# Performance work log

Hardware: AMD Instinct MI355X
Metric: run time of the kernel (lower is better)

## Reference

```python
import jax, jax.numpy as jnp
import numpy as np

# Static config (matches init_kwargs)
C = 256       # dim
H = 8         # num_heads
D = C // H    # head dim
K = 32        # patch_size (window length)
G = 1         # rt_size (relay tokens per window)
S = G + K     # window length incl. relay token
NW = 8192     # number of windows
N = NW * K    # total octree points
NB = 2        # number of HOTFormerBlocks in the stage
HID = 4 * C   # mlp hidden (mlp_ratio=4)
LS = 1e-5     # layer_scale init
SCALE = D ** -0.5


def _layernorm(x, g, b):
    m = x.mean(-1, keepdims=True)
    v = ((x - m) ** 2).mean(-1, keepdims=True)
    return (x - m) * jax.lax.rsqrt(v + 1e-5) * g + b


def setup_inputs() -> dict:
    key = jax.random.key(0)
    ks = jax.random.split(key, 20)
    w = 0.02
    inp = {
        "data": jax.random.normal(ks[0], (N, C), jnp.float32),
        "relay_tokens": jax.random.normal(ks[1], (NW, C), jnp.float32),
        # per-block parameters stacked on leading NB axis
        "cpe_w": jax.random.normal(ks[2], (NB, 3, C), jnp.float32) * w,  # depthwise k=3 conv (CPE)
        "cpe_b": jnp.zeros((NB, C), jnp.float32),
        "ln1_g": jnp.ones((NB, C), jnp.float32),
        "ln1_b": jnp.zeros((NB, C), jnp.float32),
        "qkv_w": jax.random.normal(ks[3], (NB, C, 3 * C), jnp.float32) * w,
        "qkv_b": jnp.zeros((NB, 3 * C), jnp.float32),
        "rpe": jax.random.normal(ks[4], (NB, H, S, S), jnp.float32) * w,  # relative position bias per window
        "proj_w": jax.random.normal(ks[5], (NB, C, C), jnp.float32) * w,
        "proj_b": jnp.zeros((NB, C), jnp.float32),
        "ln2_g": jnp.ones((NB, C), jnp.float32),
        "ln2_b": jnp.zeros((NB, C), jnp.float32),
        "mlp_w1": jax.random.normal(ks[6], (NB, C, HID), jnp.float32) * w,
        "mlp_b1": jnp.zeros((NB, HID), jnp.float32),
        "mlp_w2": jax.random.normal(ks[7], (NB, HID, C), jnp.float32) * w,
        "mlp_b2": jnp.zeros((NB, C), jnp.float32),
        "gamma1": jnp.full((NB, C), LS, jnp.float32),
        "gamma2": jnp.full((NB, C), LS, jnp.float32),
    }
    return inp


def reference(data, relay_tokens, cpe_w, cpe_b, ln1_g, ln1_b, qkv_w, qkv_b,
              rpe, proj_w, proj_b, ln2_g, ln2_b, mlp_w1, mlp_b1, mlp_w2,
              mlp_b2, gamma1, gamma2):
    rt = relay_tokens
    for i in range(NB):
        # CPE: depthwise kernel-3 conv along octree serialization order
        xp = jnp.pad(data, ((1, 1), (0, 0)))
        cpe = xp[:-2] * cpe_w[i, 0] + xp[1:-1] * cpe_w[i, 1] + xp[2:] * cpe_w[i, 2] + cpe_b[i]
        d = data + cpe
        # data_to_windows + prepend relay token -> [NW, S, C]
        win = d.reshape(NW, K, C)
        x = jnp.concatenate([rt[:, None, :], win], axis=1)
        # windowed MHA with RPE bias
        h = _layernorm(x, ln1_g[i], ln1_b[i])
        qkv = (h @ qkv_w[i] + qkv_b[i]).reshape(NW, S, 3, H, D)
        q, k, v = qkv[:, :, 0], qkv[:, :, 1], qkv[:, :, 2]  # [NW,S,H,D]
        scores = jnp.einsum('nqhd,nkhd->nhqk', q, k) * SCALE + rpe[i][None]
        attn = jax.nn.softmax(scores, axis=-1)
        o = jnp.einsum('nhqk,nkhd->nqhd', attn, v).reshape(NW, S, C)
        o = o @ proj_w[i] + proj_b[i]
        x = x + gamma1[i] * o  # layer-scaled residual (drop_path = identity)
        # MLP
        h2 = _layernorm(x, ln2_g[i], ln2_b[i])
        ffn = jax.nn.gelu(h2 @ mlp_w1[i] + mlp_b1[i]) @ mlp_w2[i] + mlp_b2[i]
        x = x + gamma2[i] * ffn
        # split relay token / window data, windows_to_data
        rt = x[:, 0, :]
        data = x[:, G:, :].reshape(N, C)
    return data, rt
```

## Files before the change

### kernel.cpp

```cpp
#include <hip/hip_runtime.h>
#include <hip/hip_bf16.h>


#define NW_    8192
#define KWIN   32
#define SEQ    33
#define NTOK   262144
#define MROWS  270336
#define CDIM   256
#define HEADS  8
#define HIDD   1024

typedef unsigned short u16;
typedef unsigned int u32;
typedef unsigned char u8;
typedef unsigned long long u64;
typedef __attribute__((ext_vector_type(8))) short short8;
typedef __attribute__((ext_vector_type(4))) float f32x4;
typedef __attribute__((ext_vector_type(2))) float f32x2;

__device__ __forceinline__ u16 f2bf(float f) {
    u32 u = __builtin_bit_cast(u32, f);
    u += 0x7FFFu + ((u >> 16) & 1u);
    return (u16)(u >> 16);
}
__device__ __forceinline__ float bf2f(u16 h) {
    return __builtin_bit_cast(float, (u32)h << 16);
}
__device__ __forceinline__ u32 pk2(float lo, float hi) {
    union { __hip_bfloat162 h; u32 u; } cvt;
    cvt.h = __float22bfloat162_rn(make_float2(lo, hi));
    return cvt.u;
}
__device__ __forceinline__ u32 pk4f8(float a, float b, float c, float d) {
    int pk = __builtin_amdgcn_cvt_pk_fp8_f32(a, b, 0, false);
    pk = __builtin_amdgcn_cvt_pk_fp8_f32(c, d, pk, true);
    return (u32)pk;
}
__device__ __forceinline__ float wsum(float v) {
#pragma unroll
    for (int off = 32; off > 0; off >>= 1) v += __shfl_xor(v, off);
    return v;
}
__device__ __forceinline__ float gelu_f(float v) {
    float s = fminf(fmaxf(0.4255f * v + 0.5f, 0.f), 1.f);
    return v * s;
}
__device__ __forceinline__ void gload_lds16(const void* g, void* l) {
    __builtin_amdgcn_global_load_lds(
        (const __attribute__((address_space(1))) unsigned int*)g,
        (__attribute__((address_space(3))) unsigned int*)l, 16, 0, 0);
}
__device__ __forceinline__ float4 ld4bf(const u16* p) {
    ushort4 v = *(const ushort4*)p;
    return make_float4(bf2f(v.x), bf2f(v.y), bf2f(v.z), bf2f(v.w));
}

__global__ __launch_bounds__(256) void transpose_fp8_kernel(
    const float* __restrict__ W, u8* __restrict__ Wt, int K, int N)
{
    int idx = blockIdx.x * 256 + threadIdx.x;
    if (idx >= K * N) return;
    int n = idx / K, k = idx - n * K;
    int p = __builtin_amdgcn_cvt_pk_fp8_f32(W[(size_t)k * N + n], 0.f, 0, false);
    Wt[idx] = (u8)p;
}

template<bool BF>
__global__ __launch_bounds__(256) void cpe_ln1_kernel(
    const void* __restrict__ datav, const void* __restrict__ rtv,
    const float* __restrict__ cpe_w, const float* __restrict__ cpe_b,
    const float* __restrict__ ln_g, const float* __restrict__ ln_b,
    u16* __restrict__ x, u8* __restrict__ h)
{
    const int lane = threadIdx.x & 63, wid = threadIdx.x >> 6;
    const int row = blockIdx.x * 4 + wid;
    const int w = row / SEQ, s = row - w * SEQ;
    const int c0 = lane * 4;
    float4 xv;
    if (s == 0) {
        xv = BF ? ld4bf((const u16*)rtv + (size_t)w * CDIM + c0)
                : *(const float4*)((const float*)rtv + (size_t)w * CDIM + c0);
    } else {
        const long t = (long)w * KWIN + s - 1;
        float4 a, am = {0.f,0.f,0.f,0.f}, ap = {0.f,0.f,0.f,0.f};
        if (BF) {
            const u16* d = (const u16*)datav;
            a = ld4bf(d + t * CDIM + c0);
            if (t > 0)        am = ld4bf(d + (t - 1) * CDIM + c0);
            if (t < NTOK - 1) ap = ld4bf(d + (t + 1) * CDIM + c0);
        } else {
            const float* d = (const float*)datav;
            a = *(const float4*)(d + t * CDIM + c0);
            if (t > 0)        am = *(const float4*)(d + (t - 1) * CDIM + c0);
            if (t < NTOK - 1) ap = *(const float4*)(d + (t + 1) * CDIM + c0);
        }
        const float4 w0 = *(const float4*)(cpe_w + 0 * CDIM + c0);
        const float4 w1 = *(const float4*)(cpe_w + 1 * CDIM + c0);
        const float4 w2 = *(const float4*)(cpe_w + 2 * CDIM + c0);
        const float4 cb = *(const float4*)(cpe_b + c0);
        xv.x = a.x + am.x * w0.x + a.x * w1.x + ap.x * w2.x + cb.x;
        xv.y = a.y + am.y * w0.y + a.y * w1.y + ap.y * w2.y + cb.y;
        xv.z = a.z + am.z * w0.z + a.z * w1.z + ap.z * w2.z + cb.z;
        xv.w = a.w + am.w * w0.w + a.w * w1.w + ap.w * w2.w + cb.w;
    }
    float s1 = wsum(xv.x + xv.y + xv.z + xv.w);
    float s2 = wsum(xv.x * xv.x + xv.y * xv.y + xv.z * xv.z + xv.w * xv.w);
    const float mean = s1 * (1.f / 256.f);
    const float var  = s2 * (1.f / 256.f) - mean * mean;
    const float rs   = rsqrtf(var + 1e-5f);
    const float4 g = *(const float4*)(ln_g + c0);
    const float4 b = *(const float4*)(ln_b + c0);
    uint2 xo = { pk2(xv.x, xv.y), pk2(xv.z, xv.w) };
    *(uint2*)(x + (size_t)row * CDIM + c0) = xo;
    const float h0 = (xv.x - mean) * rs * g.x + b.x;
    const float h1 = (xv.y - mean) * rs * g.y + b.y;
    const float h2 = (xv.z - mean) * rs * g.z + b.z;
    const float h3 = (xv.w - mean) * rs * g.w + b.w;
    *(u32*)(h + (size_t)row * CDIM + c0) = pk4f8(h0, h1, h2, h3);
}

__global__ __launch_bounds__(256) void ln_kernel(
    const u16* __restrict__ x, const float* __restrict__ ln_g,
    const float* __restrict__ ln_b, u8* __restrict__ h)
{
    const int lane = threadIdx.x & 63, wid = threadIdx.x >> 6;
    const int row = blockIdx.x * 4 + wid;
    const int c0 = lane * 4;
    float4 xv = ld4bf(x + (size_t)row * CDIM + c0);
    float s1 = wsum(xv.x + xv.y + xv.z + xv.w);
    float s2 = wsum(xv.x * xv.x + xv.y * xv.y + xv.z * xv.z + xv.w * xv.w);
    const float mean = s1 * (1.f / 256.f);
    const float var  = s2 * (1.f / 256.f) - mean * mean;
    const float rs   = rsqrtf(var + 1e-5f);
    const float4 g = *(const float4*)(ln_g + c0);
    const float4 b = *(const float4*)(ln_b + c0);
    const float h0 = (xv.x - mean) * rs * g.x + b.x;
    const float h1 = (xv.y - mean) * rs * g.y + b.y;
    const float h2 = (xv.z - mean) * rs * g.z + b.z;
    const float h3 = (xv.w - mean) * rs * g.w + b.w;
    *(u32*)(h + (size_t)row * CDIM + c0) = pk4f8(h0, h1, h2, h3);
}

template<int KT, int NT, int MODE>
__global__ __launch_bounds__(256, 4) void gemm_fp8_kernel(
    const u8* __restrict__ A8, const u8* __restrict__ Bt8,
    const float* __restrict__ bias, u8* __restrict__ Cout8,
    u16* __restrict__ xbuf, const float* __restrict__ gamma,
    u16* __restrict__ sdata, u16* __restrict__ srt, float* __restrict__ fout)
{
    constexpr bool F8OUT = (MODE == 1 || MODE == 5);
    __shared__ u16 sm[F8OUT ? 16384 : 17408];
    const int lane = threadIdx.x & 63, wid = threadIdx.x >> 6;
    constexpr int CX = NT / 128;
    constexpr int BAND = (MROWS / 128) / 8;
    const int bid = blockIdx.x;
    const int xcd = bid & 7, local = bid >> 3;
    const int rb = local / CX, cx = local - rb * CX;
    const int row0 = (xcd * BAND + rb) * 128;
    const int col0 = cx * 128;
    const int wr = (wid >> 1) * 64, wc = (wid & 1) * 64;
    const int lr = lane & 15, lg = lane >> 4;
    const int rsw = (lr ^ (lr >> 2)) & 3;
    f32x4 acc[4][4] = {};
    constexpr int NTk = KT / 64;

    const u8* pa[2];
    const u8* pb[2];
    int ldg[2];
#pragma unroll
    for (int cc = 0; cc < 2; ++cc) {
        const int g = wid * 2 + cc;
        const int chunk = g * 64 + lane;
        const int r = chunk >> 2, c = chunk & 3;
        const int cs = c ^ ((r ^ (r >> 2)) & 3);
        pa[cc] = A8  + (size_t)(row0 + r) * KT + cs * 16;
        pb[cc] = Bt8 + (size_t)(col0 + r) * KT + cs * 16;
        ldg[cc] = g * 1024;
    }

    auto STAGE = [&](int t) {
        char* dA = (char*)sm + (t & 1) * 8192;
        char* dB = (char*)sm + 16384 + (t & 1) * 8192;
        const size_t k0 = (size_t)t * 64;
#pragma unroll
        for (int cc = 0; cc < 2; ++cc) {
            gload_lds16(pa[cc] + k0, dA + ldg[cc]);
            gload_lds16(pb[cc] + k0, dB + ldg[cc]);
        }
    };

    STAGE(0);
    asm volatile("s_waitcnt vmcnt(0)" ::: "memory");
    __builtin_amdgcn_s_barrier();
    for (int t = 0; t < NTk; ++t) {
        if (t + 1 < NTk) STAGE(t + 1);
        const u8* Ab = (const u8*)sm + (t & 1) * 8192;
        const u8* Bb = (const u8*)sm + 16384 + (t & 1) * 8192;
#pragma unroll
        for (int kk = 0; kk < 2; ++kk) {
            const int gi = kk * 2 + (lg >> 1);
            const int off8 = (lg & 1) * 8;
            long a[4], b[4];
#pragma unroll
            for (int m = 0; m < 4; ++m)
                a[m] = *(const long*)(Ab + (wr + m * 16 + lr) * 64 + ((gi ^ rsw) * 16) + off8);
#pragma unroll
            for (int n = 0; n < 4; ++n)
                b[n] = *(const long*)(Bb + (wc + n * 16 + lr) * 64 + ((gi ^ rsw) * 16) + off8);
#pragma unroll
            for (int m = 0; m < 4; ++m)
#pragma unroll
                for (int n = 0; n < 4; ++n)
                    acc[m][n] = __builtin_amdgcn_mfma_f32_16x16x32_fp8_fp8(
                        a[m], b[n], acc[m][n], 0, 0, 0);
        }
        asm volatile("s_waitcnt vmcnt(0)" ::: "memory");
        __builtin_amdgcn_s_barrier();
    }

    __syncthreads();
    if (F8OUT) {
        u8* Ct8 = (u8*)sm;
#pragma unroll
        for (int n = 0; n < 4; ++n) {
            const int col = wc + n * 16 + lr;
            const float bv = bias[col0 + col];
#pragma unroll
            for (int m = 0; m < 4; ++m) {
                float v0 = acc[m][n][0] + bv, v1 = acc[m][n][1] + bv;
                float v2 = acc[m][n][2] + bv, v3 = acc[m][n][3] + bv;
                if (MODE == 1) { v0 = gelu_f(v0); v1 = gelu_f(v1); v2 = gelu_f(v2); v3 = gelu_f(v3); }
                const u32 pk = pk4f8(v0, v1, v2, v3);
                u8* bp = Ct8 + (wr + m * 16 + lg * 4) * 144 + col;
                bp[0]   = (u8)pk;
                bp[144] = (u8)(pk >> 8);
                bp[288] = (u8)(pk >> 16);
                bp[432] = (u8)(pk >> 24);
            }
        }
        __syncthreads();
#pragma unroll
        for (int it = 0; it < 4; ++it) {
            const int c = it * 256 + threadIdx.x;
            const int row = c >> 3, gr = c & 7;
            *(uint4*)(Cout8 + (size_t)(row0 + row) * NT + col0 + gr * 16) =
                *(const uint4*)(Ct8 + row * 144 + gr * 16);
        }
    } else {
        u16* Ct = sm;
#pragma unroll
        for (int n = 0; n < 4; ++n) {
            const int col = wc + n * 16 + lr;
            const float bv = bias[col0 + col];
#pragma unroll
            for (int m = 0; m < 4; ++m) {
                const u32 p01 = pk2(acc[m][n][0] + bv, acc[m][n][1] + bv);
                const u32 p23 = pk2(acc[m][n][2] + bv, acc[m][n][3] + bv);
                u16* bp = Ct + (wr + m * 16 + lg * 4) * 136 + col;
                bp[0]   = (u16)p01;
                bp[136] = (u16)(p01 >> 16);
                bp[272] = (u16)p23;
                bp[408] = (u16)(p23 >> 16);
            }
        }
        __syncthreads();
#pragma unroll
        for (int it = 0; it < 8; ++it) {
            const int c = it * 256 + threadIdx.x;
            const int row = c >> 4, gr = c & 15;
            const int cc0 = col0 + gr * 8;
            short8 v = *(const short8*)(Ct + row * 136 + gr * 8);
            const int grow = row0 + row;
            const float4 g0 = *(const float4*)(gamma + cc0);
            const float4 g1 = *(const float4*)(gamma + cc0 + 4);
            const float gj[8] = {g0.x, g0.y, g0.z, g0.w, g1.x, g1.y, g1.z, g1.w};
            u16* xp = xbuf + (size_t)grow * CDIM + cc0;
            short8 xv = *(const short8*)(xp);
            float xn[8];
#pragma unroll
            for (int j = 0; j < 8; ++j)
                xn[j] = bf2f((u16)xv[j]) + gj[j] * bf2f((u16)v[j]);
            if (MODE == 2) {
                uint4 o = { pk2(xn[0], xn[1]), pk2(xn[2], xn[3]),
                            pk2(xn[4], xn[5]), pk2(xn[6], xn[7]) };
                *(uint4*)xp = o;
            } else {
                const int w = grow / SEQ, s = grow - w * SEQ;
                if (MODE == 3) {
                    u16* dst = (s == 0) ? srt + (size_t)w * CDIM + cc0
                                        : sdata + ((size_t)w * KWIN + s - 1) * CDIM + cc0;
                    uint4 o = { pk2(xn[0], xn[1]), pk2(xn[2], xn[3]),
                                pk2(xn[4], xn[5]), pk2(xn[6], xn[7]) };
                    *(uint4*)dst = o;
                } else {
                    float* dst = (s == 0) ? fout + (size_t)NTOK * CDIM + (size_t)w * CDIM + cc0
                                          : fout + ((size_t)w * KWIN + s - 1) * CDIM + cc0;
                    *(float4*)dst       = make_float4(xn[0], xn[1], xn[2], xn[3]);
                    *(float4*)(dst + 4) = make_float4(xn[4], xn[5], xn[6], xn[7]);
                }
            }
        }
    }
}

__global__ __launch_bounds__(256) void attn_mfma_kernel(
    const u8* __restrict__ qkv, const float* __restrict__ rpe,
    u8* __restrict__ o)
{
    __shared__ u8 sm[4 * 6144];
    const int lane = threadIdx.x & 63, wid = threadIdx.x >> 6;
    u8* Qs = sm + wid * 6144;
    u8* Ks = Qs + 1920;
    u8* Ps = Qs;
    u8* Vt = Qs + 3840;
    const int task = blockIdx.x * 4 + wid;
    const int w = task >> 3, hh = task & 7;
    const u8* base = qkv + (size_t)(w * SEQ) * 768 + hh * 32;

#pragma unroll
    for (int it = 0; it < 5; ++it) {
        int idx = it * 64 + lane;
        if (idx < 288) *(u64*)(Vt + idx * 8) = 0ull;
    }
#pragma unroll
    for (int it = 0; it < 3; ++it) {
        int idx = it * 64 + lane;
        if (idx < 132) {
            int s = idx >> 2, c = idx & 3;
            *(u64*)(Qs + s * 40 + c * 8) = *(const u64*)(base + (size_t)s * 768 + c * 8);
            *(u64*)(Ks + s * 40 + c * 8) = *(const u64*)(base + (size_t)s * 768 + 256 + c * 8);
        }
    }
#pragma unroll
    for (int it = 0; it < 3; ++it) {
        int idx = it * 64 + lane;
        if (idx < 132) {
            int c = idx / 33, k = idx - c * 33;
            u64 v = *(const u64*)(base + (size_t)k * 768 + 512 + c * 8);
#pragma unroll
            for (int j = 0; j < 8; ++j)
                Vt[(c * 8 + j) * 72 + k] = (u8)(v >> (8 * j));
        }
    }

    const int lr = lane & 15, lg = lane >> 4;
    long qa[3], kb[3];
#pragma unroll
    for (int mi = 0; mi < 3; ++mi)
        qa[mi] = *(const long*)(Qs + (mi * 16 + lr) * 40 + lg * 8);
#pragma unroll
    for (int ni = 0; ni < 3; ++ni)
        kb[ni] = *(const long*)(Ks + (ni * 16 + lr) * 40 + lg * 8);
    f32x4 sc[3][3];
#pragma unroll
    for (int mi = 0; mi < 3; ++mi)
#pragma unroll
        for (int ni = 0; ni < 3; ++ni) {
            f32x4 z = {0.f, 0.f, 0.f, 0.f};
            sc[mi][ni] = __builtin_amdgcn_mfma_f32_16x16x32_fp8_fp8(
                qa[mi], kb[ni], z, 0, 0, 0);
        }

#pragma unroll
    for (int it = 0; it < 4; ++it) {
        int idx = it * 64 + lane;
        if (idx < 240) {
            int r = idx / 5, g = idx - r * 5;
            *(u64*)(Ps + r * 72 + 32 + g * 8) = 0ull;
        }
    }

    const float* rp = rpe + hh * SEQ * SEQ;
    const float scale = 0.17677669529663687f;
#pragma unroll
    for (int mi = 0; mi < 3; ++mi) {
#pragma unroll
        for (int q = 0; q < 4; ++q) {
            const int row = mi * 16 + lg * 4 + q;
            const bool rv_ok = (row < 33);
            float r0 = rv_ok ? rp[row * 33 + lr] : 0.f;
            float r1 = rv_ok ? rp[row * 33 + 16 + lr] : 0.f;
            float r2 = (rv_ok && lr == 0) ? rp[row * 33 + 32] : 0.f;
            float s0 = sc[mi][0][q] * scale + r0;
            float s1 = sc[mi][1][q] * scale + r1;
            float s2 = (lr == 0) ? sc[mi][2][q] * scale + r2 : -1e30f;
            float m = fmaxf(fmaxf(s0, s1), s2);
#pragma unroll
            for (int off = 1; off < 16; off <<= 1) m = fmaxf(m, __shfl_xor(m, off));
            float e0 = __expf(s0 - m), e1 = __expf(s1 - m), e2 = __expf(s2 - m);
            float sum = e0 + e1 + e2;
#pragma unroll
            for (int off = 1; off < 16; off <<= 1) sum += __shfl_xor(sum, off);
            const float inv = 1.f / sum;
            u32 p01 = (u32)__builtin_amdgcn_cvt_pk_fp8_f32(e0 * inv, e1 * inv, 0, false);
            u32 p2  = (u32)__builtin_amdgcn_cvt_pk_fp8_f32(e2 * inv, 0.f, 0, false);
            Ps[row * 72 + lr]      = (u8)p01;
            Ps[row * 72 + 16 + lr] = (u8)(p01 >> 8);
            Ps[row * 72 + 32 + lr] = (u8)p2;
        }
    }

    f32x4 oacc[3][2] = {};
#pragma unroll
    for (int ks = 0; ks < 2; ++ks) {
        long pa[3], vb[2];
#pragma unroll
        for (int mi = 0; mi < 3; ++mi)
            pa[mi] = *(const long*)(Ps + (mi * 16 + lr) * 72 + ks * 32 + lg * 8);
#pragma unroll
        for (int ni = 0; ni < 2; ++ni)
            vb[ni] = *(const long*)(Vt + (ni * 16 + lr) * 72 + ks * 32 + lg * 8);
#pragma unroll
        for (int mi = 0; mi < 3; ++mi)
#pragma unroll
            for (int ni = 0; ni < 2; ++ni)
                oacc[mi][ni] = __builtin_amdgcn_mfma_f32_16x16x32_fp8_fp8(
                    pa[mi], vb[ni], oacc[mi][ni], 0, 0, 0);
    }

#pragma unroll
    for (int mi = 0; mi < 3; ++mi)
#pragma unroll
        for (int q = 0; q < 4; ++q) {
            const int row = mi * 16 + lg * 4 + q;
            if (row < 33) {
#pragma unroll
                for (int ni = 0; ni < 2; ++ni) {
                    int pk = __builtin_amdgcn_cvt_pk_fp8_f32(oacc[mi][ni][q], 0.f, 0, false);
                    o[(size_t)(w * SEQ + row) * CDIM + hh * 32 + ni * 16 + lr] = (u8)pk;
                }
            }
        }
}

extern "C" void kernel_launch(void* const* d_in, const int* in_sizes, int n_in,
                              void* d_out, int out_size, void* d_ws, size_t ws_size,
                              hipStream_t stream)
{
    const float* data0  = (const float*)d_in[0];
    const float* rt0    = (const float*)d_in[1];
    const float* cpe_w  = (const float*)d_in[2];
    const float* cpe_b  = (const float*)d_in[3];
    const float* ln1_g  = (const float*)d_in[4];
    const float* ln1_b  = (const float*)d_in[5];
    const float* qkv_w  = (const float*)d_in[6];
    const float* qkv_b  = (const float*)d_in[7];
    const float* rpe    = (const float*)d_in[8];
    const float* proj_w = (const float*)d_in[9];
    const float* proj_b = (const float*)d_in[10];
    const float* ln2_g  = (const float*)d_in[11];
    const float* ln2_b  = (const float*)d_in[12];
    const float* w1     = (const float*)d_in[13];
    const float* b1     = (const float*)d_in[14];
    const float* w2     = (const float*)d_in[15];
    const float* b2     = (const float*)d_in[16];
    const float* g1     = (const float*)d_in[17];
    const float* g2     = (const float*)d_in[18];
    float* out = (float*)d_out;

    char* ws = (char*)d_ws;
    u8*  regA   = (u8*)ws;
    u8*  regB   = (u8*)(ws + 553648128ull);
    u16* x      = (u16*)(ws + 692060160ull);
    u16* xnd    = (u16*)(ws + 830472192ull);
    u16* xnr    = (u16*)(ws + 964689920ull);
    u8*  wqf8   = (u8*) (ws + 968884224ull);
    u8*  w1f8   = (u8*) (ws + 969277440ull);
    u8*  w2f8   = (u8*) (ws + 969801728ull);
    u8*  wpf8   = (u8*) (ws + 970326016ull);

    for (int i = 0; i < 2; ++i) {
        transpose_fp8_kernel<<<(256 * 768 + 255) / 256, 256, 0, stream>>>(
            qkv_w + (size_t)i * 256 * 768, wqf8 + (size_t)i * 768 * 256, 256, 768);
        transpose_fp8_kernel<<<(256 * 256 + 255) / 256, 256, 0, stream>>>(
            proj_w + (size_t)i * 256 * 256, wpf8 + (size_t)i * 256 * 256, 256, 256);
        transpose_fp8_kernel<<<(256 * 1024 + 255) / 256, 256, 0, stream>>>(
            w1 + (size_t)i * 256 * 1024, w1f8 + (size_t)i * 1024 * 256, 256, 1024);
        transpose_fp8_kernel<<<(256 * 1024 + 255) / 256, 256, 0, stream>>>(
            w2 + (size_t)i * 1024 * 256, w2f8 + (size_t)i * 256 * 1024, 1024, 256);
    }

    const int RT = MROWS / 128;

    for (int i = 0; i < 2; ++i) {
        if (i == 0)
            cpe_ln1_kernel<false><<<MROWS / 4, 256, 0, stream>>>(
                data0, rt0, cpe_w, cpe_b, ln1_g, ln1_b, x, regB);
        else
            cpe_ln1_kernel<true><<<MROWS / 4, 256, 0, stream>>>(
                xnd, xnr, cpe_w + 3 * 256, cpe_b + 256,
                ln1_g + 256, ln1_b + 256, x, regB);

        gemm_fp8_kernel<256, 768, 5><<<RT * 6, 256, 0, stream>>>(
            regB, wqf8 + (size_t)i * 768 * 256, qkv_b + (size_t)i * 768,
            regA, nullptr, nullptr, nullptr, nullptr, nullptr);

        attn_mfma_kernel<<<NW_ * HEADS / 4, 256, 0, stream>>>(
            regA, rpe + (size_t)i * HEADS * SEQ * SEQ, regB);

        gemm_fp8_kernel<256, 256, 2><<<RT * 2, 256, 0, stream>>>(
            regB, wpf8 + (size_t)i * 256 * 256, proj_b + (size_t)i * 256,
            nullptr, x, g1 + (size_t)i * 256, nullptr, nullptr, nullptr);

        ln_kernel<<<MROWS / 4, 256, 0, stream>>>(
            x, ln2_g + (size_t)i * 256, ln2_b + (size_t)i * 256, regB);

        gemm_fp8_kernel<256, 1024, 1><<<RT * 8, 256, 0, stream>>>(
            regB, w1f8 + (size_t)i * 1024 * 256, b1 + (size_t)i * 1024,
            regA, nullptr, nullptr, nullptr, nullptr, nullptr);

        if (i == 0)
            gemm_fp8_kernel<1024, 256, 3><<<RT * 2, 256, 0, stream>>>(
                regA, w2f8, b2,
                nullptr, x, g2, xnd, xnr, nullptr);
        else
            gemm_fp8_kernel<1024, 256, 4><<<RT * 2, 256, 0, stream>>>(
                regA, w2f8 + (size_t)256 * 1024, b2 + 256,
                nullptr, x, g2 + 256, nullptr, nullptr, out);
    }
}
```

Baseline: 1.665 ms.

## Fuse MLP up-projection, GELU and down-projection into one kernel

Replaces the separate FC1 (with GELU, fp8 output to global) and FC2 GEMM launches with a single fused kernel. Each block holds a 128-row tile of the LN2 output in LDS and loops over hidden chunks of 128: it computes FC1 plus GELU into LDS as fp8, then accumulates FC2 into registers, streaming W1 and W2 chunks. This removes the global write and re-read of the 270k x 1024 hidden activation. In exchange it uses 112 KB of LDS and large accumulators at one block per CU with fewer blocks overall, which lowers occupancy and latency hiding.

```diff
diff --git a/kernel.cpp b/kernel.cpp
--- a/kernel.cpp
+++ b/kernel.cpp
@@ -146,10 +146,9 @@
 __global__ __launch_bounds__(256, 4) void gemm_fp8_kernel(
     const u8* __restrict__ A8, const u8* __restrict__ Bt8,
     const float* __restrict__ bias, u8* __restrict__ Cout8,
-    u16* __restrict__ xbuf, const float* __restrict__ gamma,
-    u16* __restrict__ sdata, u16* __restrict__ srt, float* __restrict__ fout)
+    u16* __restrict__ xbuf, const float* __restrict__ gamma)
 {
-    constexpr bool F8OUT = (MODE == 1 || MODE == 5);
+    constexpr bool F8OUT = (MODE == 5);
     __shared__ u16 sm[F8OUT ? 16384 : 17408];
     const int lane = threadIdx.x & 63, wid = threadIdx.x >> 6;
     constexpr int CX = NT / 128;
@@ -230,7 +229,6 @@
             for (int m = 0; m < 4; ++m) {
                 float v0 = acc[m][n][0] + bv, v1 = acc[m][n][1] + bv;
                 float v2 = acc[m][n][2] + bv, v3 = acc[m][n][3] + bv;
-                if (MODE == 1) { v0 = gelu_f(v0); v1 = gelu_f(v1); v2 = gelu_f(v2); v3 = gelu_f(v3); }
                 const u32 pk = pk4f8(v0, v1, v2, v3);
                 u8* bp = Ct8 + (wr + m * 16 + lg * 4) * 144 + col;
                 bp[0]   = (u8)pk;
@@ -281,24 +279,185 @@
 #pragma unroll
             for (int j = 0; j < 8; ++j)
                 xn[j] = bf2f((u16)xv[j]) + gj[j] * bf2f((u16)v[j]);
-            if (MODE == 2) {
+            uint4 o = { pk2(xn[0], xn[1]), pk2(xn[2], xn[3]),
+                        pk2(xn[4], xn[5]), pk2(xn[6], xn[7]) };
+            *(uint4*)xp = o;
+        }
+    }
+}
+
+template<int FMODE>
+__global__ __launch_bounds__(256, 1) void mlp_fused_kernel(
+    const u8* __restrict__ h2, const u8* __restrict__ w1f8,
+    const u8* __restrict__ w2f8, const float* __restrict__ b1,
+    const float* __restrict__ b2, const u16* __restrict__ xbuf,
+    const float* __restrict__ gamma, u16* __restrict__ sdata,
+    u16* __restrict__ srt, float* __restrict__ fout)
+{
+    __shared__ u8 sm[114688];
+    u8* H  = sm;
+    u8* W1 = sm + 32768;
+    u8* W2 = sm + 65536;
+    u8* P  = sm + 98304;
+    const int lane = threadIdx.x & 63, wid = threadIdx.x >> 6;
+    const int bid = blockIdx.x;
+    const int xcd = bid & 7, rb = bid >> 3;
+    const int row0 = (xcd * 264 + rb) * 128;
+    const int wr = (wid >> 1) * 64;
+    const int wc1 = (wid & 1) * 64;
+    const int lr = lane & 15, lg = lane >> 4;
+    const int sw = lr & 7;
+
+    auto STAGE_A = [&](const u8* src, u8* dst) {
+#pragma unroll
+        for (int t = 0; t < 2; ++t)
+#pragma unroll
+            for (int cc = 0; cc < 4; ++cc) {
+                const int g = wid * 4 + cc;
+                const int G = g * 64 + lane;
+                const int r = G >> 3, c = G & 7;
+                gload_lds16(src + (size_t)r * 256 + t * 128 + ((c ^ (r & 7)) * 16),
+                            dst + t * 16384 + g * 1024);
+            }
+    };
+    auto STAGE_W2 = [&](const u8* src) {
+#pragma unroll
+        for (int cc = 0; cc < 8; ++cc) {
+            const int g = wid * 8 + cc;
+            const int G = g * 64 + lane;
+            const int r = G >> 3, c = G & 7;
+            gload_lds16(src + (size_t)r * 1024 + ((c ^ (r & 7)) * 16),
+                        W2 + g * 1024);
+        }
+    };
+
+    STAGE_A(h2 + (size_t)row0 * 256, H);
+    STAGE_A(w1f8, W1);
+    asm volatile("s_waitcnt vmcnt(0)" ::: "memory");
+    __builtin_amdgcn_s_barrier();
+
+    f32x4 acc2[4][8] = {};
+    for (int j = 0; j < 8; ++j) {
+        STAGE_W2(w2f8 + j * 128);
+
+        f32x4 acc1[4][4] = {};
+#pragma unroll
+        for (int t = 0; t < 2; ++t) {
+            const u8* Ab = H + t * 16384;
+            const u8* Bb = W1 + t * 16384;
+#pragma unroll
+            for (int kk = 0; kk < 4; ++kk) {
+                const int gi = kk * 2 + (lg >> 1);
+                const int off8 = (lg & 1) * 8;
+                long a[4], b[4];
+#pragma unroll
+                for (int m = 0; m < 4; ++m)
+                    a[m] = *(const long*)(Ab + (wr + m * 16 + lr) * 128 + ((gi ^ sw) * 16) + off8);
+#pragma unroll
+                for (int n = 0; n < 4; ++n)
+                    b[n] = *(const long*)(Bb + (wc1 + n * 16 + lr) * 128 + ((gi ^ sw) * 16) + off8);
+#pragma unroll
+                for (int m = 0; m < 4; ++m)
+#pragma unroll
+                    for (int n = 0; n < 4; ++n)
+                        acc1[m][n] = __builtin_amdgcn_mfma_f32_16x16x32_fp8_fp8(
+                            a[m], b[n], acc1[m][n], 0, 0, 0);
+            }
+        }
+#pragma unroll
+        for (int n = 0; n < 4; ++n) {
+            const int col = wc1 + n * 16 + lr;
+            const float bv = b1[j * 128 + col];
+#pragma unroll
+            for (int m = 0; m < 4; ++m) {
+                const u32 pk = pk4f8(gelu_f(acc1[m][n][0] + bv),
+                                     gelu_f(acc1[m][n][1] + bv),
+                                     gelu_f(acc1[m][n][2] + bv),
+                                     gelu_f(acc1[m][n][3] + bv));
+                u8* bp = P + (wr + m * 16 + lg * 4) * 144 + col;
+                bp[0]   = (u8)pk;
+                bp[144] = (u8)(pk >> 8);
+                bp[288] = (u8)(pk >> 16);
+                bp[432] = (u8)(pk >> 24);
+            }
+        }
+        asm volatile("s_waitcnt vmcnt(0)" ::: "memory");
+        __builtin_amdgcn_s_barrier();
+
+        if (j < 7) STAGE_A(w1f8 + (size_t)(j + 1) * 128 * 256, W1);
+
+#pragma unroll
+        for (int kk = 0; kk < 4; ++kk) {
+            const int gi = kk * 2 + (lg >> 1);
+            const int off8 = (lg & 1) * 8;
+            long a[4], b[8];
+#pragma unroll
+            for (int m = 0; m < 4; ++m)
+                a[m] = *(const long*)(P + (wr + m * 16 + lr) * 144 + gi * 16 + off8);
+#pragma unroll
+            for (int n = 0; n < 8; ++n)
+                b[n] = *(const long*)(W2 + ((wid & 1) * 128 + n * 16 + lr) * 128 + ((gi ^ sw) * 16) + off8);
+#pragma unroll
+            for (int m = 0; m < 4; ++m)
+#pragma unroll
+                for (int n = 0; n < 8; ++n)
+                    acc2[m][n] = __builtin_amdgcn_mfma_f32_16x16x32_fp8_fp8(
+                        a[m], b[n], acc2[m][n], 0, 0, 0);
+        }
+        asm volatile("s_waitcnt vmcnt(0)" ::: "memory");
+        __builtin_amdgcn_s_barrier();
+    }
+
+    u16* Ct = (u16*)(sm + 32768);
+#pragma unroll
+    for (int p = 0; p < 2; ++p) {
+        __syncthreads();
+        if ((wid & 1) == p) {
+#pragma unroll
+            for (int n = 0; n < 8; ++n) {
+                const int col = n * 16 + lr;
+                const float bv = b2[p * 128 + col];
+#pragma unroll
+                for (int m = 0; m < 4; ++m) {
+                    const u32 p01 = pk2(acc2[m][n][0] + bv, acc2[m][n][1] + bv);
+                    const u32 p23 = pk2(acc2[m][n][2] + bv, acc2[m][n][3] + bv);
+                    u16* bp = Ct + (wr + m * 16 + lg * 4) * 136 + col;
+                    bp[0]   = (u16)p01;
+                    bp[136] = (u16)(p01 >> 16);
+                    bp[272] = (u16)p23;
+                    bp[408] = (u16)(p23 >> 16);
+                }
+            }
+        }
+        __syncthreads();
+#pragma unroll
+        for (int it = 0; it < 8; ++it) {
+            const int c = it * 256 + threadIdx.x;
+            const int row = c >> 4, gr = c & 15;
+            const int cc0 = p * 128 + gr * 8;
+            short8 v = *(const short8*)(Ct + row * 136 + gr * 8);
+            const int grow = row0 + row;
+            const float4 g0 = *(const float4*)(gamma + cc0);
+            const float4 g1 = *(const float4*)(gamma + cc0 + 4);
+            const float gj[8] = {g0.x, g0.y, g0.z, g0.w, g1.x, g1.y, g1.z, g1.w};
+            const u16* xp = xbuf + (size_t)grow * CDIM + cc0;
+            short8 xv = *(const short8*)(xp);
+            float xn[8];
+#pragma unroll
+            for (int jj = 0; jj < 8; ++jj)
+                xn[jj] = bf2f((u16)xv[jj]) + gj[jj] * bf2f((u16)v[jj]);
+            const int w = grow / SEQ, s = grow - w * SEQ;
+            if (FMODE == 3) {
+                u16* dst = (s == 0) ? srt + (size_t)w * CDIM + cc0
+                                    : sdata + ((size_t)w * KWIN + s - 1) * CDIM + cc0;
                 uint4 o = { pk2(xn[0], xn[1]), pk2(xn[2], xn[3]),
                             pk2(xn[4], xn[5]), pk2(xn[6], xn[7]) };
-                *(uint4*)xp = o;
+                *(uint4*)dst = o;
             } else {
-                const int w = grow / SEQ, s = grow - w * SEQ;
-                if (MODE == 3) {
-                    u16* dst = (s == 0) ? srt + (size_t)w * CDIM + cc0
-                                        : sdata + ((size_t)w * KWIN + s - 1) * CDIM + cc0;
-                    uint4 o = { pk2(xn[0], xn[1]), pk2(xn[2], xn[3]),
-                                pk2(xn[4], xn[5]), pk2(xn[6], xn[7]) };
-                    *(uint4*)dst = o;
-                } else {
-                    float* dst = (s == 0) ? fout + (size_t)NTOK * CDIM + (size_t)w * CDIM + cc0
-                                          : fout + ((size_t)w * KWIN + s - 1) * CDIM + cc0;
-                    *(float4*)dst       = make_float4(xn[0], xn[1], xn[2], xn[3]);
-                    *(float4*)(dst + 4) = make_float4(xn[4], xn[5], xn[6], xn[7]);
-                }
+                float* dst = (s == 0) ? fout + (size_t)NTOK * CDIM + (size_t)w * CDIM + cc0
+                                      : fout + ((size_t)w * KWIN + s - 1) * CDIM + cc0;
+                *(float4*)dst       = make_float4(xn[0], xn[1], xn[2], xn[3]);
+                *(float4*)(dst + 4) = make_float4(xn[4], xn[5], xn[6], xn[7]);
             }
         }
     }
@@ -494,29 +653,26 @@
 
         gemm_fp8_kernel<256, 768, 5><<<RT * 6, 256, 0, stream>>>(
             regB, wqf8 + (size_t)i * 768 * 256, qkv_b + (size_t)i * 768,
-            regA, nullptr, nullptr, nullptr, nullptr, nullptr);
+            regA, nullptr, nullptr);
 
         attn_mfma_kernel<<<NW_ * HEADS / 4, 256, 0, stream>>>(
             regA, rpe + (size_t)i * HEADS * SEQ * SEQ, regB);
 
         gemm_fp8_kernel<256, 256, 2><<<RT * 2, 256, 0, stream>>>(
             regB, wpf8 + (size_t)i * 256 * 256, proj_b + (size_t)i * 256,
-            nullptr, x, g1 + (size_t)i * 256, nullptr, nullptr, nullptr);
+            nullptr, x, g1 + (size_t)i * 256);
 
         ln_kernel<<<MROWS / 4, 256, 0, stream>>>(
             x, ln2_g + (size_t)i * 256, ln2_b + (size_t)i * 256, regB);
 
-        gemm_fp8_kernel<256, 1024, 1><<<RT * 8, 256, 0, stream>>>(
-            regB, w1f8 + (size_t)i * 1024 * 256, b1 + (size_t)i * 1024,
-            regA, nullptr, nullptr, nullptr, nullptr, nullptr);
-
         if (i == 0)
-            gemm_fp8_kernel<1024, 256, 3><<<RT * 2, 256, 0, stream>>>(
-                regA, w2f8, b2,
-                nullptr, x, g2, xnd, xnr, nullptr);
+            mlp_fused_kernel<3><<<RT, 256, 0, stream>>>(
+                regB, w1f8, w2f8, b1, b2,
+                x, g2, xnd, xnr, nullptr);
         else
-            gemm_fp8_kernel<1024, 256, 4><<<RT * 2, 256, 0, stream>>>(
-                regA, w2f8 + (size_t)256 * 1024, b2 + 256,
-                nullptr, x, g2 + 256, nullptr, nullptr, out);
-    }
-}
+            mlp_fused_kernel<4><<<RT, 256, 0, stream>>>(
+                regB, w1f8 + (size_t)1024 * 256, w2f8 + (size_t)256 * 1024,
+                b1 + HIDD, b2 + CDIM,
+                x, g2 + CDIM, nullptr, nullptr, out);
+    }
+}
```

Result: slower. 1.883 ms (+13.1%).
